# Kernel tuning notes

Hardware: AMD Instinct MI355X
Metric: run time of the kernel (lower is better)

Reference implementation:

```python
import jax, jax.numpy as jnp
import numpy as np

B, L, D, E, K, P = 1024, 320, 128, 8, 2, 96
NOISE_EPS = 0.01
LOSS_COEF = 0.01


def setup_inputs() -> dict:
    key = jax.random.key(0)
    ks = jax.random.split(key, 8)
    return {
        "x": jax.random.normal(ks[0], (B, L, D), jnp.float32),
        "x_mark_enc": jax.random.normal(ks[1], (B, L, 4), jnp.float32),
        "noise": jax.random.normal(ks[2], (B, E), jnp.float32),  # randn_like in torch
        "start_w": jax.random.normal(ks[3], (D, 1), jnp.float32) * 0.05,
        "start_b": jnp.zeros((1,), jnp.float32),
        "w_gate": jax.random.normal(ks[4], (L, E), jnp.float32) * 0.02,
        "w_noise": jax.random.normal(ks[5], (L, E), jnp.float32) * 0.02,
        "expert_w": jax.random.normal(ks[6], (E, L, P), jnp.float32) * (1.0 / np.sqrt(L)),
        "expert_b": jnp.zeros((E, P, D), jnp.float32),
    }


def _norm_cdf(v):
    return 0.5 * (1.0 + jax.lax.erf(v * (1.0 / np.sqrt(2.0)).astype(v.dtype) if hasattr((1.0 / np.sqrt(2.0)), 'astype') else v / jnp.sqrt(jnp.asarray(2.0, v.dtype))))


def _cdf(v):
    # standard normal CDF, Normal(0,1).cdf
    return 0.5 * (1.0 + jax.lax.erf(v / jnp.sqrt(jnp.asarray(2.0, v.dtype))))


def _cv_squared(v):
    eps = 1e-10
    return jnp.var(v, ddof=1) / (jnp.mean(v) ** 2 + eps)


def reference(x, x_mark_enc, noise, start_w, start_b, w_gate, w_noise, expert_b, expert_w):
    # --- noisy top-k gating (train mode) ---
    g = jnp.squeeze(x @ start_w, -1) + start_b  # [B, L]
    clean_logits = g @ w_gate                    # [B, E]
    noise_std = jax.nn.softplus(g @ w_noise) + NOISE_EPS
    noisy_logits = clean_logits + noise * noise_std

    top_logits, top_idx = jax.lax.top_k(noisy_logits, K + 1)  # [B, K+1]
    top_k_gates = jax.nn.softmax(top_logits[:, :K], axis=1)
    gates = jnp.zeros_like(noisy_logits).at[
        jnp.arange(noisy_logits.shape[0])[:, None], top_idx[:, :K]
    ].set(top_k_gates)  # [B, E] sparse gates (zeros elsewhere)

    # --- differentiable load via prob-in-top-k ---
    thr_in = top_logits[:, K:K + 1]       # (k+1)-th noisy value
    thr_out = top_logits[:, K - 1:K]      # k-th noisy value
    clean_c = jnp.where(jnp.isnan(clean_logits), 0.0, clean_logits)
    prob = jnp.where(
        noisy_logits > thr_in,
        _cdf((clean_c - thr_in) / noise_std),
        _cdf((clean_c - thr_out) / noise_std),
    )
    load = prob.sum(0)          # [E]
    importance = gates.sum(0)   # [E]
    balance_loss = LOSS_COEF * (_cv_squared(importance) + _cv_squared(load))

    # --- dispatch/combine: dense-equivalent of SparseDispatcher ---
    # expert e: out_e = einsum('bld,lp->bpd', x, W_e); combine weights = gates
    per_expert = jnp.einsum('bld,elp->ebpd', x, expert_w)          # [E, B, P, D]
    out = jnp.einsum('be,ebpd->bpd', gates, per_expert)
    out = out + jnp.einsum('be,epd->bpd', gates, expert_b)
    regu_sum = jnp.asarray(0.0, jnp.float32)
    return out, balance_loss, regu_sum
```

## Files before the change

### kernel.cpp

```cpp
#include <hip/hip_runtime.h>
#include <hip/hip_bf16.h>

#define Bn 1024
#define Lr 320
#define Dd 128
#define Ee 8
#define Pp 96

typedef short bf16x8 __attribute__((ext_vector_type(8)));
typedef float f32x4 __attribute__((ext_vector_type(4)));
typedef unsigned short u16;

__device__ __forceinline__ float cdf_f(float v) {
    return 0.5f * (1.0f + erff(v * 0.70710678118654752f));
}
__device__ __forceinline__ float softplus_f(float x) {
    return fmaxf(x, 0.0f) + log1pf(expf(-fabsf(x)));
}
__device__ __forceinline__ u16 f2bf(float f) {
    unsigned int u = __float_as_uint(f);
    return (u16)((u + 0x7fffu + ((u >> 16) & 1u)) >> 16);
}
__device__ __forceinline__ float bf2f(u16 u) {
    return __uint_as_float(((unsigned int)u) << 16);
}

__global__ __launch_bounds__(256) void transpose_w(
    const float* __restrict__ ew, u16* __restrict__ wt)
{
    __shared__ float tile[Pp * 33];
    const int e  = blockIdx.x;
    const int l0 = blockIdx.y * 32;
    const int t  = threadIdx.x;
    #pragma unroll
    for (int i = 0; i < 12; ++i) {
        const int idx = t + 256 * i;
        const int lp = idx / 96, p = idx - 96 * lp;
        tile[p * 33 + lp] = ew[((size_t)e * Lr + l0 + lp) * Pp + p];
    }
    __syncthreads();
    #pragma unroll
    for (int i = 0; i < 6; ++i) {
        const int g = t + 256 * i;
        const int p = g >> 4, l2 = (g & 15) * 2;
        const unsigned pk = (unsigned)f2bf(tile[p * 33 + l2]) |
                            ((unsigned)f2bf(tile[p * 33 + l2 + 1]) << 16);
        *(unsigned*)&wt[((size_t)(e * Pp + p)) * Lr + l0 + l2] = pk;
    }
}

__global__ __launch_bounds__(256, 4) void fused_kernel(
    const float* __restrict__ x, const float* __restrict__ noise,
    const float* __restrict__ start_w, const float* __restrict__ start_b,
    const float* __restrict__ w_gate, const float* __restrict__ w_noise,
    const u16* __restrict__ wt, const float* __restrict__ expert_b,
    float* __restrict__ accum, float* __restrict__ out)
{
    __shared__ float g_s[Lr];
    __shared__ float pc_s[256], pn_s[256];
    __shared__ float cl_s[Ee], sd_s[Ee], ns_s[Ee], gt_s[Ee];
    __shared__ float thr_s[2];
    __shared__ __align__(16) u16 Xs[Dd * 40];
    __shared__ __align__(16) u16 Ws[Pp * 40];

    const int b    = blockIdx.x;
    const int tid  = threadIdx.x;
    const int lane = tid & 63;
    const int wv   = tid >> 6;
    const int hl   = lane & 31;
    const float* xb = x + (size_t)b * Lr * Dd;

    {
        const float4 swv = ((const float4*)start_w)[hl];
        const float  sb  = start_b[0];
        for (int p = wv; p < Lr / 2; p += 4) {
            const int row = 2 * p + (lane >> 5);
            const float4 xv = ((const float4*)(xb + row * Dd))[hl];
            float part = xv.x * swv.x + xv.y * swv.y + xv.z * swv.z + xv.w * swv.w;
            #pragma unroll
            for (int off = 16; off >= 1; off >>= 1) part += __shfl_xor(part, off);
            if (hl == 0) g_s[row] = part + sb;
        }
        __syncthreads();
        {
            const int e = tid & 7, j = tid >> 3;
            float pc = 0.f, pn = 0.f;
            for (int l = j; l < Lr; l += 32) {
                const float gvv = g_s[l];
                pc += gvv * w_gate[l * Ee + e];
                pn += gvv * w_noise[l * Ee + e];
            }
            pc_s[tid] = pc; pn_s[tid] = pn;
        }
        __syncthreads();
        if (tid < Ee) {
            float c = 0.f, nv = 0.f;
            for (int jj = 0; jj < 32; ++jj) { c += pc_s[tid + 8 * jj]; nv += pn_s[tid + 8 * jj]; }
            const float sdv = softplus_f(nv) + 0.01f;
            cl_s[tid] = c;
            sd_s[tid] = sdv;
            ns_s[tid] = c + noise[b * Ee + tid] * sdv;
            gt_s[tid] = 0.f;
        }
        __syncthreads();
        if (tid == 0) {
            float v[Ee];
            #pragma unroll
            for (int i = 0; i < Ee; ++i) v[i] = ns_s[i];
            int i0 = -1, i1 = -1;
            float v0 = -INFINITY, v1 = -INFINITY, v2 = -INFINITY;
            for (int i = 0; i < Ee; ++i) if (v[i] > v0) { v0 = v[i]; i0 = i; }
            for (int i = 0; i < Ee; ++i) if (i != i0 && v[i] > v1) { v1 = v[i]; i1 = i; }
            for (int i = 0; i < Ee; ++i) if (i != i0 && i != i1 && v[i] > v2) { v2 = v[i]; }
            const float ex1 = expf(v1 - v0);
            const float den = 1.f + ex1;
            gt_s[i0] = 1.f / den;
            gt_s[i1] = ex1 / den;
            thr_s[0] = v2;
            thr_s[1] = v1;
        }
        __syncthreads();
        if (tid < Ee) {
            const float gvv = gt_s[tid];
            atomicAdd(&accum[8 + tid], gvv);
            float c = cl_s[tid];
            if (isnan(c)) c = 0.f;
            const float sdv = sd_s[tid];
            const float pr = (ns_s[tid] > thr_s[0]) ? cdf_f((c - thr_s[0]) / sdv)
                                                    : cdf_f((c - thr_s[1]) / sdv);
            atomicAdd(&accum[tid], pr);
        }
        __syncthreads();
    }

    int e0 = 0, e1 = 0; float g0 = 0.f, g1 = 0.f;
    {
        int cnt = 0;
        #pragma unroll
        for (int e = 0; e < Ee; ++e) {
            const float gv = gt_s[e];
            if (gv != 0.f) {
                if (cnt == 0) { e0 = e; g0 = gv; }
                else if (cnt == 1) { e1 = e; g1 = gv; }
                ++cnt;
            }
        }
    }

    const int quad  = lane >> 4;
    const int r16   = lane & 15;
    const int dbase = 32 * wv;
    const int dcol  = tid & 127;
    const int lgrp  = tid >> 7;

    f32x4 acc[6][2];
    #pragma unroll
    for (int m = 0; m < 6; ++m)
        #pragma unroll
        for (int n = 0; n < 2; ++n) acc[m][n] = (f32x4){0.f, 0.f, 0.f, 0.f};

    for (int l0 = 0; l0 < Lr; l0 += 32) {
        #pragma unroll
        for (int k = 0; k < 8; ++k) {
            const int lp = 16 * lgrp + 2 * k;
            const float a = xb[(size_t)(l0 + lp) * Dd + dcol];
            const float c = xb[(size_t)(l0 + lp + 1) * Dd + dcol];
            ((unsigned*)Xs)[(dcol * 40 + lp) >> 1] =
                (unsigned)f2bf(a) | ((unsigned)f2bf(c) << 16);
        }
        #pragma unroll
        for (int i = 0; i < 3; ++i) {
            const int g = tid + 256 * i;
            const int p = g >> 3, lq = (g & 7) * 4;
            const ushort4 w0 = *(const ushort4*)&wt[(size_t)(e0 * Pp + p) * Lr + l0 + lq];
            const ushort4 w1 = *(const ushort4*)&wt[(size_t)(e1 * Pp + p) * Lr + l0 + lq];
            ushort4 o;
            o.x = f2bf(g0 * bf2f(w0.x) + g1 * bf2f(w1.x));
            o.y = f2bf(g0 * bf2f(w0.y) + g1 * bf2f(w1.y));
            o.z = f2bf(g0 * bf2f(w0.z) + g1 * bf2f(w1.z));
            o.w = f2bf(g0 * bf2f(w0.w) + g1 * bf2f(w1.w));
            *(ushort4*)&Ws[p * 40 + lq] = o;
        }
        __syncthreads();
        bf16x8 af[6], bfr[2];
        #pragma unroll
        for (int m = 0; m < 6; ++m)
            af[m] = *(const bf16x8*)&Ws[(16 * m + r16) * 40 + 8 * quad];
        #pragma unroll
        for (int n = 0; n < 2; ++n)
            bfr[n] = *(const bf16x8*)&Xs[(dbase + 16 * n + r16) * 40 + 8 * quad];
        #pragma unroll
        for (int m = 0; m < 6; ++m)
            #pragma unroll
            for (int n = 0; n < 2; ++n)
                acc[m][n] = __builtin_amdgcn_mfma_f32_16x16x32_bf16(
                    af[m], bfr[n], acc[m][n], 0, 0, 0);
        __syncthreads();
    }

    const float* eb0 = expert_b + (size_t)e0 * Pp * Dd;
    const float* eb1 = expert_b + (size_t)e1 * Pp * Dd;
    #pragma unroll
    for (int m = 0; m < 6; ++m) {
        #pragma unroll
        for (int n = 0; n < 2; ++n) {
            const int d = dbase + 16 * n + r16;
            #pragma unroll
            for (int r = 0; r < 4; ++r) {
                const int p = 16 * m + 4 * quad + r;
                out[((size_t)b * Pp + p) * Dd + d] =
                    acc[m][n][r] + g0 * eb0[p * Dd + d] + g1 * eb1[p * Dd + d];
            }
        }
    }
}

__global__ void loss_kernel(const float* __restrict__ accum,
                            float* __restrict__ out_scalars)
{
    if (threadIdx.x == 0) {
        float lo[8], im[8];
        #pragma unroll
        for (int i = 0; i < 8; ++i) { lo[i] = accum[i]; im[i] = accum[8 + i]; }
        float ml = 0.f, mi = 0.f;
        #pragma unroll
        for (int i = 0; i < 8; ++i) { ml += lo[i]; mi += im[i]; }
        ml *= 0.125f; mi *= 0.125f;
        float sl = 0.f, si = 0.f;
        #pragma unroll
        for (int i = 0; i < 8; ++i) {
            const float dl = lo[i] - ml, di = im[i] - mi;
            sl += dl * dl; si += di * di;
        }
        const float cvl = (sl / 7.f) / (ml * ml + 1e-10f);
        const float cvi = (si / 7.f) / (mi * mi + 1e-10f);
        out_scalars[0] = 0.01f * (cvi + cvl);
        out_scalars[1] = 0.0f;
    }
}

extern "C" void kernel_launch(void* const* d_in, const int* in_sizes, int n_in,
                              void* d_out, int out_size, void* d_ws, size_t ws_size,
                              hipStream_t stream)
{
    const float* x        = (const float*)d_in[0];
    const float* noise    = (const float*)d_in[2];
    const float* start_w  = (const float*)d_in[3];
    const float* start_b  = (const float*)d_in[4];
    const float* w_gate   = (const float*)d_in[5];
    const float* w_noise  = (const float*)d_in[6];
    const float* expert_w = (const float*)d_in[7];
    const float* expert_b = (const float*)d_in[8];
    float* out            = (float*)d_out;

    float* accum = (float*)d_ws;
    u16*   wt    = (u16*)((char*)d_ws + 256);

    hipMemsetAsync(accum, 0, 16 * sizeof(float), stream);
    hipLaunchKernelGGL(transpose_w, dim3(Ee, Lr / 32), dim3(256), 0, stream,
                       expert_w, wt);
    hipLaunchKernelGGL(fused_kernel, dim3(Bn), dim3(256), 0, stream,
                       x, noise, start_w, start_b, w_gate, w_noise,
                       wt, expert_b, accum, out);
    hipLaunchKernelGGL(loss_kernel, dim3(1), dim3(64), 0, stream,
                       accum, out + (size_t)Bn * Pp * Dd);
}
```

Baseline: 321.5 us.

## Split fused MoE kernel into g, gating, and matmul kernels

```diff
diff --git a/kernel.cpp b/kernel.cpp
--- a/kernel.cpp
+++ b/kernel.cpp
@@ -49,168 +49,186 @@
     }
 }
 
-__global__ __launch_bounds__(256, 4) void fused_kernel(
-    const float* __restrict__ x, const float* __restrict__ noise,
-    const float* __restrict__ start_w, const float* __restrict__ start_b,
+__global__ __launch_bounds__(256, 8) void g_kernel(
+    const float* __restrict__ x, const float* __restrict__ start_w,
+    const float* __restrict__ start_b, float* __restrict__ g_out)
+{
+    const int t  = threadIdx.x;
+    const int lc = blockIdx.x;
+    const int b  = blockIdx.y;
+    const float sb = start_b[0];
+
+    float4 sw[4];
+    #pragma unroll
+    for (int j = 0; j < 4; ++j) sw[j] = ((const float4*)start_w)[(t & 7) + 8 * j];
+
+    const float* xb = x + ((size_t)b * Lr + lc * 64) * Dd;
+    #pragma unroll
+    for (int p2 = 0; p2 < 2; ++p2) {
+        const int r = p2 * 32 + (t >> 3);
+        float acc = 0.f;
+        #pragma unroll
+        for (int j = 0; j < 4; ++j) {
+            const float4 v = ((const float4*)(xb + (size_t)r * Dd))[(t & 7) + 8 * j];
+            acc += v.x * sw[j].x + v.y * sw[j].y + v.z * sw[j].z + v.w * sw[j].w;
+        }
+        #pragma unroll
+        for (int off = 1; off <= 4; off <<= 1) acc += __shfl_xor(acc, off);
+        if ((t & 7) == 0) g_out[(size_t)b * Lr + lc * 64 + r] = acc + sb;
+    }
+}
+
+__global__ __launch_bounds__(256) void gate_kernel(
+    const float* __restrict__ g, const float* __restrict__ noise,
     const float* __restrict__ w_gate, const float* __restrict__ w_noise,
-    const u16* __restrict__ wt, const float* __restrict__ expert_b,
-    float* __restrict__ accum, float* __restrict__ out)
-{
-    __shared__ float g_s[Lr];
-    __shared__ float pc_s[256], pn_s[256];
-    __shared__ float cl_s[Ee], sd_s[Ee], ns_s[Ee], gt_s[Ee];
-    __shared__ float thr_s[2];
-    __shared__ __align__(16) u16 Xs[Dd * 40];
-    __shared__ __align__(16) u16 Ws[Pp * 40];
-
-    const int b    = blockIdx.x;
-    const int tid  = threadIdx.x;
+    float* __restrict__ accum, float* __restrict__ gates_out)
+{
+    __shared__ float sred[16];
+    const int t    = threadIdx.x;
+    const int lane = t & 63;
+    const int wv   = t >> 6;
+    const int b    = blockIdx.x * 4 + wv;
+
+    if (t < 16) sred[t] = 0.f;
+    __syncthreads();
+
+    const int e = lane & 7, seg = lane >> 3;
+    const float* gb = g + (size_t)b * Lr;
+    float pc = 0.f, pn = 0.f;
+    #pragma unroll 8
+    for (int i = 0; i < 40; ++i) {
+        const int l = seg * 40 + i;
+        const float gv = gb[l];
+        pc += gv * w_gate[l * Ee + e];
+        pn += gv * w_noise[l * Ee + e];
+    }
+    #pragma unroll
+    for (int off = 8; off <= 32; off <<= 1) {
+        pc += __shfl_xor(pc, off);
+        pn += __shfl_xor(pn, off);
+    }
+    const float sdv   = softplus_f(pn) + 0.01f;
+    float       c     = pc;
+    const float nz    = noise[b * Ee + e];
+    const float noisy = c + nz * sdv;
+
+    float nv[8];
+    #pragma unroll
+    for (int j = 0; j < 8; ++j) nv[j] = __shfl(noisy, j);
+
+    int i0 = -1, i1 = -1;
+    float v0 = -INFINITY, v1 = -INFINITY, v2 = -INFINITY;
+    #pragma unroll
+    for (int i = 0; i < 8; ++i) if (nv[i] > v0) { v0 = nv[i]; i0 = i; }
+    #pragma unroll
+    for (int i = 0; i < 8; ++i) if (i != i0 && nv[i] > v1) { v1 = nv[i]; i1 = i; }
+    #pragma unroll
+    for (int i = 0; i < 8; ++i) if (i != i0 && i != i1 && nv[i] > v2) { v2 = nv[i]; }
+
+    const float ex1 = expf(v1 - v0);
+    const float den = 1.f + ex1;
+    const float gate_e = (e == i0) ? (1.f / den) : ((e == i1) ? (ex1 / den) : 0.f);
+
+    if (isnan(c)) c = 0.f;
+    const float pr = (noisy > v2) ? cdf_f((c - v2) / sdv) : cdf_f((c - v1) / sdv);
+
+    if (lane < 8) {
+        gates_out[b * Ee + e] = gate_e;
+        atomicAdd(&sred[8 + e], gate_e);
+        atomicAdd(&sred[e], pr);
+    }
+    __syncthreads();
+    if (t < 16) atomicAdd(&accum[t], sred[t]);
+}
+
+__global__ __launch_bounds__(256, 4) void mm_kernel(
+    const float* __restrict__ x, const u16* __restrict__ wt,
+    const float* __restrict__ expert_b, const float* __restrict__ gates,
+    float* __restrict__ out)
+{
+    __shared__ __align__(16) u16 Xs[64 * 34];
+    __shared__ __align__(16) u16 Ws[Pp * 34];
+
+    const int b   = blockIdx.x >> 1;
+    const int h   = blockIdx.x & 1;
+    const int tid = threadIdx.x;
     const int lane = tid & 63;
     const int wv   = tid >> 6;
-    const int hl   = lane & 31;
-    const float* xb = x + (size_t)b * Lr * Dd;
-
-    {
-        const float4 swv = ((const float4*)start_w)[hl];
-        const float  sb  = start_b[0];
-        for (int p = wv; p < Lr / 2; p += 4) {
-            const int row = 2 * p + (lane >> 5);
-            const float4 xv = ((const float4*)(xb + row * Dd))[hl];
-            float part = xv.x * swv.x + xv.y * swv.y + xv.z * swv.z + xv.w * swv.w;
-            #pragma unroll
-            for (int off = 16; off >= 1; off >>= 1) part += __shfl_xor(part, off);
-            if (hl == 0) g_s[row] = part + sb;
-        }
-        __syncthreads();
-        {
-            const int e = tid & 7, j = tid >> 3;
-            float pc = 0.f, pn = 0.f;
-            for (int l = j; l < Lr; l += 32) {
-                const float gvv = g_s[l];
-                pc += gvv * w_gate[l * Ee + e];
-                pn += gvv * w_noise[l * Ee + e];
-            }
-            pc_s[tid] = pc; pn_s[tid] = pn;
-        }
-        __syncthreads();
-        if (tid < Ee) {
-            float c = 0.f, nv = 0.f;
-            for (int jj = 0; jj < 32; ++jj) { c += pc_s[tid + 8 * jj]; nv += pn_s[tid + 8 * jj]; }
-            const float sdv = softplus_f(nv) + 0.01f;
-            cl_s[tid] = c;
-            sd_s[tid] = sdv;
-            ns_s[tid] = c + noise[b * Ee + tid] * sdv;
-            gt_s[tid] = 0.f;
-        }
-        __syncthreads();
-        if (tid == 0) {
-            float v[Ee];
-            #pragma unroll
-            for (int i = 0; i < Ee; ++i) v[i] = ns_s[i];
-            int i0 = -1, i1 = -1;
-            float v0 = -INFINITY, v1 = -INFINITY, v2 = -INFINITY;
-            for (int i = 0; i < Ee; ++i) if (v[i] > v0) { v0 = v[i]; i0 = i; }
-            for (int i = 0; i < Ee; ++i) if (i != i0 && v[i] > v1) { v1 = v[i]; i1 = i; }
-            for (int i = 0; i < Ee; ++i) if (i != i0 && i != i1 && v[i] > v2) { v2 = v[i]; }
-            const float ex1 = expf(v1 - v0);
-            const float den = 1.f + ex1;
-            gt_s[i0] = 1.f / den;
-            gt_s[i1] = ex1 / den;
-            thr_s[0] = v2;
-            thr_s[1] = v1;
-        }
-        __syncthreads();
-        if (tid < Ee) {
-            const float gvv = gt_s[tid];
-            atomicAdd(&accum[8 + tid], gvv);
-            float c = cl_s[tid];
-            if (isnan(c)) c = 0.f;
-            const float sdv = sd_s[tid];
-            const float pr = (ns_s[tid] > thr_s[0]) ? cdf_f((c - thr_s[0]) / sdv)
-                                                    : cdf_f((c - thr_s[1]) / sdv);
-            atomicAdd(&accum[tid], pr);
-        }
-        __syncthreads();
-    }
-
-    int e0 = 0, e1 = 0; float g0 = 0.f, g1 = 0.f;
-    {
-        int cnt = 0;
-        #pragma unroll
-        for (int e = 0; e < Ee; ++e) {
-            const float gv = gt_s[e];
-            if (gv != 0.f) {
-                if (cnt == 0) { e0 = e; g0 = gv; }
-                else if (cnt == 1) { e1 = e; g1 = gv; }
-                ++cnt;
-            }
-        }
-    }
-
-    const int quad  = lane >> 4;
-    const int r16   = lane & 15;
-    const int dbase = 32 * wv;
-    const int dcol  = tid & 127;
-    const int lgrp  = tid >> 7;
-
-    f32x4 acc[6][2];
-    #pragma unroll
-    for (int m = 0; m < 6; ++m)
-        #pragma unroll
-        for (int n = 0; n < 2; ++n) acc[m][n] = (f32x4){0.f, 0.f, 0.f, 0.f};
+    const int quad = lane >> 4;
+    const int r16  = lane & 15;
+
+    int e0 = 0, e1 = 0; float g0 = 0.f, g1 = 0.f; int cnt = 0;
+    #pragma unroll
+    for (int e = 0; e < Ee; ++e) {
+        const float gv = gates[b * Ee + e];
+        if (gv != 0.f) {
+            if (cnt == 0) { e0 = e; g0 = gv; }
+            else if (cnt == 1) { e1 = e; g1 = gv; }
+            ++cnt;
+        }
+    }
+
+    f32x4 acc[6];
+    #pragma unroll
+    for (int m = 0; m < 6; ++m) acc[m] = (f32x4){0.f, 0.f, 0.f, 0.f};
+
+    const float* xb = x + (size_t)b * Lr * Dd + h * 64;
+    const int dloc = tid & 63;
+    const int lg   = tid >> 6;
 
     for (int l0 = 0; l0 < Lr; l0 += 32) {
         #pragma unroll
-        for (int k = 0; k < 8; ++k) {
-            const int lp = 16 * lgrp + 2 * k;
-            const float a = xb[(size_t)(l0 + lp) * Dd + dcol];
-            const float c = xb[(size_t)(l0 + lp + 1) * Dd + dcol];
-            ((unsigned*)Xs)[(dcol * 40 + lp) >> 1] =
-                (unsigned)f2bf(a) | ((unsigned)f2bf(c) << 16);
-        }
-        #pragma unroll
         for (int i = 0; i < 3; ++i) {
-            const int g = tid + 256 * i;
-            const int p = g >> 3, lq = (g & 7) * 4;
+            const int gi = tid + 256 * i;
+            const int p = gi >> 3, lq = (gi & 7) * 4;
             const ushort4 w0 = *(const ushort4*)&wt[(size_t)(e0 * Pp + p) * Lr + l0 + lq];
             const ushort4 w1 = *(const ushort4*)&wt[(size_t)(e1 * Pp + p) * Lr + l0 + lq];
-            ushort4 o;
-            o.x = f2bf(g0 * bf2f(w0.x) + g1 * bf2f(w1.x));
-            o.y = f2bf(g0 * bf2f(w0.y) + g1 * bf2f(w1.y));
-            o.z = f2bf(g0 * bf2f(w0.z) + g1 * bf2f(w1.z));
-            o.w = f2bf(g0 * bf2f(w0.w) + g1 * bf2f(w1.w));
-            *(ushort4*)&Ws[p * 40 + lq] = o;
+            const unsigned lo = (unsigned)f2bf(g0 * bf2f(w0.x) + g1 * bf2f(w1.x)) |
+                                ((unsigned)f2bf(g0 * bf2f(w0.y) + g1 * bf2f(w1.y)) << 16);
+            const unsigned hi = (unsigned)f2bf(g0 * bf2f(w0.z) + g1 * bf2f(w1.z)) |
+                                ((unsigned)f2bf(g0 * bf2f(w0.w) + g1 * bf2f(w1.w)) << 16);
+            ((unsigned*)Ws)[p * 17 + (lq >> 1)]     = lo;
+            ((unsigned*)Ws)[p * 17 + (lq >> 1) + 1] = hi;
+        }
+        {
+            float v[8];
+            #pragma unroll
+            for (int k = 0; k < 8; ++k)
+                v[k] = xb[(size_t)(l0 + lg * 8 + k) * Dd + dloc];
+            #pragma unroll
+            for (int k2 = 0; k2 < 4; ++k2) {
+                const unsigned pk = (unsigned)f2bf(v[2 * k2]) |
+                                    ((unsigned)f2bf(v[2 * k2 + 1]) << 16);
+                ((unsigned*)Xs)[dloc * 17 + lg * 4 + k2] = pk;
+            }
         }
         __syncthreads();
-        bf16x8 af[6], bfr[2];
-        #pragma unroll
-        for (int m = 0; m < 6; ++m)
-            af[m] = *(const bf16x8*)&Ws[(16 * m + r16) * 40 + 8 * quad];
-        #pragma unroll
-        for (int n = 0; n < 2; ++n)
-            bfr[n] = *(const bf16x8*)&Xs[(dbase + 16 * n + r16) * 40 + 8 * quad];
-        #pragma unroll
-        for (int m = 0; m < 6; ++m)
+        union U { unsigned u[4]; bf16x8 v; };
+        U bfr;
+        #pragma unroll
+        for (int cW = 0; cW < 4; ++cW)
+            bfr.u[cW] = ((const unsigned*)Xs)[(16 * wv + r16) * 17 + 4 * quad + cW];
+        #pragma unroll
+        for (int m = 0; m < 6; ++m) {
+            U af;
             #pragma unroll
-            for (int n = 0; n < 2; ++n)
-                acc[m][n] = __builtin_amdgcn_mfma_f32_16x16x32_bf16(
-                    af[m], bfr[n], acc[m][n], 0, 0, 0);
+            for (int cW = 0; cW < 4; ++cW)
+                af.u[cW] = ((const unsigned*)Ws)[(16 * m + r16) * 17 + 4 * quad + cW];
+            acc[m] = __builtin_amdgcn_mfma_f32_16x16x32_bf16(af.v, bfr.v, acc[m], 0, 0, 0);
+        }
         __syncthreads();
     }
 
+    const int d = h * 64 + 16 * wv + r16;
     const float* eb0 = expert_b + (size_t)e0 * Pp * Dd;
     const float* eb1 = expert_b + (size_t)e1 * Pp * Dd;
     #pragma unroll
     for (int m = 0; m < 6; ++m) {
         #pragma unroll
-        for (int n = 0; n < 2; ++n) {
-            const int d = dbase + 16 * n + r16;
-            #pragma unroll
-            for (int r = 0; r < 4; ++r) {
-                const int p = 16 * m + 4 * quad + r;
-                out[((size_t)b * Pp + p) * Dd + d] =
-                    acc[m][n][r] + g0 * eb0[p * Dd + d] + g1 * eb1[p * Dd + d];
-            }
+        for (int r = 0; r < 4; ++r) {
+            const int p = 16 * m + 4 * quad + r;
+            out[((size_t)b * Pp + p) * Dd + d] =
+                acc[m][r] + g0 * eb0[p * Dd + d] + g1 * eb1[p * Dd + d];
         }
     }
 }
@@ -254,14 +272,19 @@
     float* out            = (float*)d_out;
 
     float* accum = (float*)d_ws;
-    u16*   wt    = (u16*)((char*)d_ws + 256);
+    float* gates = accum + 16;
+    float* gbuf  = gates + Bn * Ee;
+    u16*   wt    = (u16*)(gbuf + Bn * Lr);
 
     hipMemsetAsync(accum, 0, 16 * sizeof(float), stream);
     hipLaunchKernelGGL(transpose_w, dim3(Ee, Lr / 32), dim3(256), 0, stream,
                        expert_w, wt);
-    hipLaunchKernelGGL(fused_kernel, dim3(Bn), dim3(256), 0, stream,
-                       x, noise, start_w, start_b, w_gate, w_noise,
-                       wt, expert_b, accum, out);
+    hipLaunchKernelGGL(g_kernel, dim3(5, Bn), dim3(256), 0, stream,
+                       x, start_w, start_b, gbuf);
+    hipLaunchKernelGGL(gate_kernel, dim3(Bn / 4), dim3(256), 0, stream,
+                       gbuf, noise, w_gate, w_noise, accum, gates);
+    hipLaunchKernelGGL(mm_kernel, dim3(Bn * 2), dim3(256), 0, stream,
+                       x, wt, expert_b, gates, out);
     hipLaunchKernelGGL(loss_kernel, dim3(1), dim3(64), 0, stream,
                        accum, out + (size_t)Bn * Pp * Dd);
 }
```

Measured after the change: 316.0 us. Within noise of the previous version (-1.7%).
